# Performance work log

Hardware: AMD Instinct MI355X
Metric: run time of the kernel (lower is better)

## Reference

```python
import jax, jax.numpy as jnp
import numpy as np

N, NEMB, NHID, NCLASS = 8192, 128, 64, 16
NEG_SLOPE = 0.2
NEG_INF = -1e9


def setup_inputs() -> dict:
    key = jax.random.key(0)
    ks = jax.random.split(key, 10)
    x = jax.random.normal(ks[0], (N, NEMB), dtype=jnp.float32)
    adj = (jax.random.uniform(ks[1], (N, N)) < 0.01).astype(jnp.float32)
    adj = jnp.maximum(adj, jnp.eye(N, dtype=jnp.float32))
    s = 1.0 / np.sqrt(NHID)
    W1 = jax.random.uniform(ks[2], (NEMB, NHID), minval=-s, maxval=s, dtype=jnp.float32)
    a1_src = jax.random.uniform(ks[3], (NHID,), minval=-s, maxval=s, dtype=jnp.float32)
    a1_dst = jax.random.uniform(ks[4], (NHID,), minval=-s, maxval=s, dtype=jnp.float32)
    b1 = jnp.zeros((NHID,), dtype=jnp.float32)
    s2 = 1.0 / np.sqrt(NCLASS)
    W2 = jax.random.uniform(ks[5], (NHID, NCLASS), minval=-s2, maxval=s2, dtype=jnp.float32)
    a2_src = jax.random.uniform(ks[6], (NCLASS,), minval=-s2, maxval=s2, dtype=jnp.float32)
    a2_dst = jax.random.uniform(ks[7], (NCLASS,), minval=-s2, maxval=s2, dtype=jnp.float32)
    b2 = jnp.zeros((NCLASS,), dtype=jnp.float32)
    return {"x": x, "adj": adj, "W1": W1, "a1_src": a1_src, "a1_dst": a1_dst,
            "b1": b1, "W2": W2, "a2_src": a2_src, "a2_dst": a2_dst, "b2": b2}


def gat_conv(x, adj_mask, W, a_src, a_dst, b):
    # h: [N, F']
    h = x @ W
    # e_ij = LeakyReLU(a_src . h_i + a_dst . h_j), masked softmax over neighbors j
    alpha_src = h @ a_src  # [N]
    alpha_dst = h @ a_dst  # [N]
    e = jax.nn.leaky_relu(alpha_src[:, None] + alpha_dst[None, :], NEG_SLOPE)
    e = jnp.where(adj_mask, e, NEG_INF)
    attn = jax.nn.softmax(e, axis=-1)  # [N, N]
    out = attn @ h + b
    return jax.nn.elu(out)


def reference(x, adj, W1, a1_src, a1_dst, b1, W2, a2_src, a2_dst, b2):
    mask = adj > 0
    h = gat_conv(x, mask, W1, a1_src, a1_dst, b1)
    out = gat_conv(h, mask, W2, a2_src, a2_dst, b2)
    return out
```

## Files before the change

### kernel.cpp

```cpp
#include <hip/hip_runtime.h>
#include <math.h>

#define NN 8192
#define NEMBD 128
#define NHID 64
#define NCLS 16
#define MAXN 256
#define NEG_SLOPE 0.2f

typedef float f4 __attribute__((ext_vector_type(4)));

__device__ __forceinline__ float wave_max64(float v) {
    v = fmaxf(v, __shfl_xor(v, 1));
    v = fmaxf(v, __shfl_xor(v, 2));
    v = fmaxf(v, __shfl_xor(v, 4));
    v = fmaxf(v, __shfl_xor(v, 8));
    v = fmaxf(v, __shfl_xor(v, 16));
    v = fmaxf(v, __shfl_xor(v, 32));
    return v;
}
__device__ __forceinline__ float wave_sum64(float v) {
    v += __shfl_xor(v, 1);
    v += __shfl_xor(v, 2);
    v += __shfl_xor(v, 4);
    v += __shfl_xor(v, 8);
    v += __shfl_xor(v, 16);
    v += __shfl_xor(v, 32);
    return v;
}

__global__ __launch_bounds__(256) void k1_scan_h1(
    const float* __restrict__ adj, const float* __restrict__ x,
    const float* __restrict__ W1,
    const float* __restrict__ a1s, const float* __restrict__ a1d,
    float* __restrict__ h1, float* __restrict__ als, float* __restrict__ ald,
    int* __restrict__ g_cnt, int* __restrict__ g_nbr) {
    __shared__ int s_idx[4][MAXN];
    int wid = threadIdx.x >> 6, lane = threadIdx.x & 63;
    int row = blockIdx.x * 4 + wid;
    const f4* arow = (const f4*)(adj + (size_t)row * NN);
    const float* xr = x + (size_t)row * NEMBD;
    unsigned long long lt = (1ull << lane) - 1ull;
    int base = 0;
    float hacc = 0.f;
    for (int it = 0; it < NN / 256; ++it) {
        f4 v = __builtin_nontemporal_load(arow + it * 64 + lane);
#pragma unroll
        for (int s = 0; s < 4; ++s) {
            int k = it * 4 + s;
            hacc = fmaf(xr[k], W1[k * NHID + lane], hacc);
        }
#pragma unroll
        for (int s = 0; s < 4; ++s) {
            bool nz = v[s] > 0.f;
            unsigned long long m = __ballot(nz);
            if (nz) {
                int pos = base + __popcll(m & lt);
                if (pos < MAXN) s_idx[wid][pos] = it * 256 + lane * 4 + s;
            }
            base += __popcll(m);
        }
    }
    int cnt = base < MAXN ? base : MAXN;
    if (lane == 0) g_cnt[row] = cnt;
    for (int n = lane; n < cnt; n += 64)
        g_nbr[(size_t)row * MAXN + n] = s_idx[wid][n];
    h1[(size_t)row * NHID + lane] = hacc;
    float ts = wave_sum64(hacc * a1s[lane]);
    float td = wave_sum64(hacc * a1d[lane]);
    if (lane == 0) { als[row] = ts; ald[row] = td; }
}

__global__ __launch_bounds__(256) void k2_attn1_h2(
    const float* __restrict__ h1, const float* __restrict__ als,
    const float* __restrict__ ald, const float* __restrict__ b1,
    const float* __restrict__ W2, const float* __restrict__ a2s,
    const float* __restrict__ a2d,
    const int* __restrict__ g_cnt, const int* __restrict__ g_nbr,
    float* __restrict__ h2, float* __restrict__ als2, float* __restrict__ ald2) {
    __shared__ int   s_idx[4][MAXN];
    __shared__ float s_p[4][MAXN];
    __shared__ float s_h[4][NHID];
    int wid = threadIdx.x >> 6, lane = threadIdx.x & 63;
    int row = blockIdx.x * 4 + wid;
    int cnt = g_cnt[row];
    for (int n = lane; n < cnt; n += 64) s_idx[wid][n] = g_nbr[(size_t)row * MAXN + n];

    float asrow = als[row];
    float mloc = -1e30f;
    for (int n = lane; n < cnt; n += 64) {
        float e = asrow + ald[s_idx[wid][n]];
        e = e > 0.f ? e : NEG_SLOPE * e;
        s_p[wid][n] = e;
        mloc = fmaxf(mloc, e);
    }
    float mrow = wave_max64(mloc);
    float ssum = 0.f;
    for (int n = lane; n < cnt; n += 64) {
        float p = __expf(s_p[wid][n] - mrow);
        s_p[wid][n] = p;
        ssum += p;
    }
    float rinv = 1.f / wave_sum64(ssum);

    int c4 = lane & 15, kk = lane >> 4;
    f4 acc = {0.f, 0.f, 0.f, 0.f};
#pragma unroll 4
    for (int n = kk; n < cnt; n += 4) {
        float p = s_p[wid][n];
        f4 v = ((const f4*)(h1 + (size_t)s_idx[wid][n] * NHID))[c4];
        acc.x = fmaf(p, v.x, acc.x);
        acc.y = fmaf(p, v.y, acc.y);
        acc.z = fmaf(p, v.z, acc.z);
        acc.w = fmaf(p, v.w, acc.w);
    }
    acc.x += __shfl_xor(acc.x, 16); acc.y += __shfl_xor(acc.y, 16);
    acc.z += __shfl_xor(acc.z, 16); acc.w += __shfl_xor(acc.w, 16);
    acc.x += __shfl_xor(acc.x, 32); acc.y += __shfl_xor(acc.y, 32);
    acc.z += __shfl_xor(acc.z, 32); acc.w += __shfl_xor(acc.w, 32);
    if (kk == 0) {
        f4 o;
#pragma unroll
        for (int j = 0; j < 4; ++j) {
            float t = acc[j] * rinv + b1[c4 * 4 + j];
            o[j] = t > 0.f ? t : expm1f(t);
        }
        ((f4*)s_h[wid])[c4] = o;
    }
    __builtin_amdgcn_s_barrier();

    int c = lane & 15, k = lane >> 4;
    float a2 = 0.f;
#pragma unroll
    for (int f = k * 16; f < k * 16 + 16; ++f)
        a2 = fmaf(s_h[wid][f], W2[f * NCLS + c], a2);
    a2 += __shfl_xor(a2, 16);
    a2 += __shfl_xor(a2, 32);
    if (lane < 16) h2[(size_t)row * NCLS + lane] = a2;
    float ts = a2 * a2s[c], td = a2 * a2d[c];
    ts += __shfl_xor(ts, 1); td += __shfl_xor(td, 1);
    ts += __shfl_xor(ts, 2); td += __shfl_xor(td, 2);
    ts += __shfl_xor(ts, 4); td += __shfl_xor(td, 4);
    ts += __shfl_xor(ts, 8); td += __shfl_xor(td, 8);
    if (lane == 0) { als2[row] = ts; ald2[row] = td; }
}

__global__ __launch_bounds__(256) void k3_attn2(
    const float* __restrict__ h2, const float* __restrict__ als2,
    const float* __restrict__ ald2, const float* __restrict__ b2,
    const int* __restrict__ g_cnt, const int* __restrict__ g_nbr,
    float* __restrict__ out) {
    __shared__ int   s_idx[4][MAXN];
    __shared__ float s_p[4][MAXN];
    int wid = threadIdx.x >> 6, lane = threadIdx.x & 63;
    int row = blockIdx.x * 4 + wid;
    int cnt = g_cnt[row];
    for (int n = lane; n < cnt; n += 64) s_idx[wid][n] = g_nbr[(size_t)row * MAXN + n];

    float asrow = als2[row];
    float mloc = -1e30f;
    for (int n = lane; n < cnt; n += 64) {
        float e = asrow + ald2[s_idx[wid][n]];
        e = e > 0.f ? e : NEG_SLOPE * e;
        s_p[wid][n] = e;
        mloc = fmaxf(mloc, e);
    }
    float mrow = wave_max64(mloc);
    float ssum = 0.f;
    for (int n = lane; n < cnt; n += 64) {
        float p = __expf(s_p[wid][n] - mrow);
        s_p[wid][n] = p;
        ssum += p;
    }
    float rinv = 1.f / wave_sum64(ssum);

    int c4 = lane & 3, kk = lane >> 2;
    f4 acc = {0.f, 0.f, 0.f, 0.f};
#pragma unroll 2
    for (int n = kk; n < cnt; n += 16) {
        float p = s_p[wid][n];
        f4 v = ((const f4*)(h2 + (size_t)s_idx[wid][n] * NCLS))[c4];
        acc.x = fmaf(p, v.x, acc.x);
        acc.y = fmaf(p, v.y, acc.y);
        acc.z = fmaf(p, v.z, acc.z);
        acc.w = fmaf(p, v.w, acc.w);
    }
#pragma unroll
    for (int d = 4; d <= 32; d <<= 1) {
        acc.x += __shfl_xor(acc.x, d); acc.y += __shfl_xor(acc.y, d);
        acc.z += __shfl_xor(acc.z, d); acc.w += __shfl_xor(acc.w, d);
    }
    if (kk == 0) {
        f4 o;
#pragma unroll
        for (int j = 0; j < 4; ++j) {
            float t = acc[j] * rinv + b2[c4 * 4 + j];
            o[j] = t > 0.f ? t : expm1f(t);
        }
        ((f4*)(out + (size_t)row * NCLS))[c4] = o;
    }
}

extern "C" void kernel_launch(void* const* d_in, const int* in_sizes, int n_in,
                              void* d_out, int out_size, void* d_ws, size_t ws_size,
                              hipStream_t stream) {
    const float* x   = (const float*)d_in[0];
    const float* adj = (const float*)d_in[1];
    const float* W1  = (const float*)d_in[2];
    const float* a1s = (const float*)d_in[3];
    const float* a1d = (const float*)d_in[4];
    const float* b1  = (const float*)d_in[5];
    const float* W2  = (const float*)d_in[6];
    const float* a2s = (const float*)d_in[7];
    const float* a2d = (const float*)d_in[8];
    const float* b2  = (const float*)d_in[9];
    float* out = (float*)d_out;

    char* ws = (char*)d_ws;
    float* h1   = (float*)(ws + 0);
    float* h2v  = (float*)(ws + 2097152);
    float* als1 = (float*)(ws + 2621440);
    float* ald1 = (float*)(ws + 2654208);
    float* als2 = (float*)(ws + 2686976);
    float* ald2 = (float*)(ws + 2719744);
    int*   gcnt = (int*)  (ws + 2752512);
    int*   gnbr = (int*)  (ws + 2785280);

    dim3 blk(256);
    dim3 grid(NN / 4);
    k1_scan_h1 <<<grid, blk, 0, stream>>>(adj, x, W1, a1s, a1d, h1, als1, ald1, gcnt, gnbr);
    k2_attn1_h2<<<grid, blk, 0, stream>>>(h1, als1, ald1, b1, W2, a2s, a2d, gcnt, gnbr,
                                          h2v, als2, ald2);
    k3_attn2   <<<grid, blk, 0, stream>>>(h2v, als2, ald2, b2, gcnt, gnbr, out);
}
```

Before: 81.06 us.

## Fuse adjacency scan with layer-1 attention and software-pipeline rows per wave

The h1 projection moves into its own small kernel. The adjacency scan is fused with the layer-1 attention and the h2 projection, and each wave now handles 4 rows. While the wave scans one row's adjacency with prefetched chunks, it interleaves the gather-accumulate for the previous row, using double-buffered shared neighbor and probability lists. The aim is to hide the latency of gathering h1 rows behind the 256 MB adjacency stream and to drop one kernel's worth of index reloads. The cost is fewer blocks (512), which may lower the memory parallelism available for streaming the adjacency.

```diff
diff --git a/kernel.cpp b/kernel.cpp
--- a/kernel.cpp
+++ b/kernel.cpp
@@ -7,6 +7,8 @@
 #define NCLS 16
 #define MAXN 256
 #define NEG_SLOPE 0.2f
+#define WPB 4
+#define RPW 4
 
 typedef float f4 __attribute__((ext_vector_type(4)));
 
@@ -29,120 +31,187 @@
     return v;
 }
 
-__global__ __launch_bounds__(256) void k1_scan_h1(
-    const float* __restrict__ adj, const float* __restrict__ x,
-    const float* __restrict__ W1,
+__global__ __launch_bounds__(256) void kA_h1(
+    const float* __restrict__ x, const float* __restrict__ W1,
     const float* __restrict__ a1s, const float* __restrict__ a1d,
-    float* __restrict__ h1, float* __restrict__ als, float* __restrict__ ald,
-    int* __restrict__ g_cnt, int* __restrict__ g_nbr) {
-    __shared__ int s_idx[4][MAXN];
+    float* __restrict__ h1, float* __restrict__ als, float* __restrict__ ald) {
     int wid = threadIdx.x >> 6, lane = threadIdx.x & 63;
     int row = blockIdx.x * 4 + wid;
-    const f4* arow = (const f4*)(adj + (size_t)row * NN);
     const float* xr = x + (size_t)row * NEMBD;
+    float acc = 0.f;
+#pragma unroll 8
+    for (int k = 0; k < NEMBD; ++k)
+        acc = fmaf(xr[k], W1[k * NHID + lane], acc);
+    h1[(size_t)row * NHID + lane] = acc;
+    float ts = wave_sum64(acc * a1s[lane]);
+    float td = wave_sum64(acc * a1d[lane]);
+    if (lane == 0) { als[row] = ts; ald[row] = td; }
+}
+
+__global__ __launch_bounds__(256) void kB_fused(
+    const float* __restrict__ adj, const float* __restrict__ h1,
+    const float* __restrict__ als, const float* __restrict__ ald,
+    const float* __restrict__ b1, const float* __restrict__ W2,
+    const float* __restrict__ a2s, const float* __restrict__ a2d,
+    int* __restrict__ g_cnt, int* __restrict__ g_nbr,
+    float* __restrict__ h2, float* __restrict__ als2, float* __restrict__ ald2) {
+    __shared__ int   S_idx[WPB][2][MAXN];
+    __shared__ float S_p[WPB][2][MAXN];
+    __shared__ float S_h[WPB][NHID];
+    int wid = threadIdx.x >> 6, lane = threadIdx.x & 63;
+    int row0 = (blockIdx.x * WPB + wid) * RPW;
     unsigned long long lt = (1ull << lane) - 1ull;
-    int base = 0;
-    float hacc = 0.f;
-    for (int it = 0; it < NN / 256; ++it) {
-        f4 v = __builtin_nontemporal_load(arow + it * 64 + lane);
-#pragma unroll
-        for (int s = 0; s < 4; ++s) {
-            int k = it * 4 + s;
-            hacc = fmaf(xr[k], W1[k * NHID + lane], hacc);
-        }
-#pragma unroll
-        for (int s = 0; s < 4; ++s) {
-            bool nz = v[s] > 0.f;
-            unsigned long long m = __ballot(nz);
-            if (nz) {
-                int pos = base + __popcll(m & lt);
-                if (pos < MAXN) s_idx[wid][pos] = it * 256 + lane * 4 + s;
-            }
-            base += __popcll(m);
-        }
-    }
-    int cnt = base < MAXN ? base : MAXN;
-    if (lane == 0) g_cnt[row] = cnt;
-    for (int n = lane; n < cnt; n += 64)
-        g_nbr[(size_t)row * MAXN + n] = s_idx[wid][n];
-    h1[(size_t)row * NHID + lane] = hacc;
-    float ts = wave_sum64(hacc * a1s[lane]);
-    float td = wave_sum64(hacc * a1d[lane]);
-    if (lane == 0) { als[row] = ts; ald[row] = td; }
-}
-
-__global__ __launch_bounds__(256) void k2_attn1_h2(
-    const float* __restrict__ h1, const float* __restrict__ als,
-    const float* __restrict__ ald, const float* __restrict__ b1,
-    const float* __restrict__ W2, const float* __restrict__ a2s,
-    const float* __restrict__ a2d,
-    const int* __restrict__ g_cnt, const int* __restrict__ g_nbr,
-    float* __restrict__ h2, float* __restrict__ als2, float* __restrict__ ald2) {
-    __shared__ int   s_idx[4][MAXN];
-    __shared__ float s_p[4][MAXN];
-    __shared__ float s_h[4][NHID];
-    int wid = threadIdx.x >> 6, lane = threadIdx.x & 63;
-    int row = blockIdx.x * 4 + wid;
-    int cnt = g_cnt[row];
-    for (int n = lane; n < cnt; n += 64) s_idx[wid][n] = g_nbr[(size_t)row * MAXN + n];
-
-    float asrow = als[row];
-    float mloc = -1e30f;
-    for (int n = lane; n < cnt; n += 64) {
-        float e = asrow + ald[s_idx[wid][n]];
-        e = e > 0.f ? e : NEG_SLOPE * e;
-        s_p[wid][n] = e;
-        mloc = fmaxf(mloc, e);
-    }
-    float mrow = wave_max64(mloc);
-    float ssum = 0.f;
-    for (int n = lane; n < cnt; n += 64) {
-        float p = __expf(s_p[wid][n] - mrow);
-        s_p[wid][n] = p;
-        ssum += p;
-    }
-    float rinv = 1.f / wave_sum64(ssum);
-
     int c4 = lane & 15, kk = lane >> 4;
+
+    int pcnt = 0, prow = -1;
+    float prinv = 0.f;
     f4 acc = {0.f, 0.f, 0.f, 0.f};
-#pragma unroll 4
-    for (int n = kk; n < cnt; n += 4) {
-        float p = s_p[wid][n];
-        f4 v = ((const f4*)(h1 + (size_t)s_idx[wid][n] * NHID))[c4];
-        acc.x = fmaf(p, v.x, acc.x);
-        acc.y = fmaf(p, v.y, acc.y);
-        acc.z = fmaf(p, v.z, acc.z);
-        acc.w = fmaf(p, v.w, acc.w);
-    }
-    acc.x += __shfl_xor(acc.x, 16); acc.y += __shfl_xor(acc.y, 16);
-    acc.z += __shfl_xor(acc.z, 16); acc.w += __shfl_xor(acc.w, 16);
-    acc.x += __shfl_xor(acc.x, 32); acc.y += __shfl_xor(acc.y, 32);
-    acc.z += __shfl_xor(acc.z, 32); acc.w += __shfl_xor(acc.w, 32);
-    if (kk == 0) {
-        f4 o;
-#pragma unroll
-        for (int j = 0; j < 4; ++j) {
-            float t = acc[j] * rinv + b1[c4 * 4 + j];
-            o[j] = t > 0.f ? t : expm1f(t);
-        }
-        ((f4*)s_h[wid])[c4] = o;
-    }
-    __builtin_amdgcn_s_barrier();
-
-    int c = lane & 15, k = lane >> 4;
-    float a2 = 0.f;
-#pragma unroll
-    for (int f = k * 16; f < k * 16 + 16; ++f)
-        a2 = fmaf(s_h[wid][f], W2[f * NCLS + c], a2);
-    a2 += __shfl_xor(a2, 16);
-    a2 += __shfl_xor(a2, 32);
-    if (lane < 16) h2[(size_t)row * NCLS + lane] = a2;
-    float ts = a2 * a2s[c], td = a2 * a2d[c];
-    ts += __shfl_xor(ts, 1); td += __shfl_xor(td, 1);
-    ts += __shfl_xor(ts, 2); td += __shfl_xor(td, 2);
-    ts += __shfl_xor(ts, 4); td += __shfl_xor(td, 4);
-    ts += __shfl_xor(ts, 8); td += __shfl_xor(td, 8);
-    if (lane == 0) { als2[row] = ts; ald2[row] = td; }
+
+#pragma unroll 1
+    for (int r = 0; r < RPW; ++r) {
+        int row = row0 + r;
+        int buf = r & 1, pb = buf ^ 1;
+        const f4* arow = (const f4*)(adj + (size_t)row * NN);
+        int base = 0;
+        f4 cur0 = __builtin_nontemporal_load(arow + 0 * 64 + lane);
+        f4 cur1 = __builtin_nontemporal_load(arow + 1 * 64 + lane);
+        f4 cur2 = __builtin_nontemporal_load(arow + 2 * 64 + lane);
+        f4 cur3 = __builtin_nontemporal_load(arow + 3 * 64 + lane);
+
+#pragma unroll 1
+        for (int c = 0; c < 8; ++c) {
+            if (r > 0) {
+                int lo = (pcnt * c) >> 3, hi = (pcnt * (c + 1)) >> 3;
+#pragma unroll 2
+                for (int n = lo + kk; n < hi; n += 4) {
+                    float p = S_p[wid][pb][n];
+                    int j = S_idx[wid][pb][n];
+                    f4 v = ((const f4*)(h1 + (size_t)j * NHID))[c4];
+                    acc.x = fmaf(p, v.x, acc.x);
+                    acc.y = fmaf(p, v.y, acc.y);
+                    acc.z = fmaf(p, v.z, acc.z);
+                    acc.w = fmaf(p, v.w, acc.w);
+                }
+            }
+            f4 n0 = {0,0,0,0}, n1 = {0,0,0,0}, n2 = {0,0,0,0}, n3 = {0,0,0,0};
+            if (c < 7) {
+                const f4* p = arow + (c + 1) * 256 + lane;
+                n0 = __builtin_nontemporal_load(p + 0 * 64);
+                n1 = __builtin_nontemporal_load(p + 1 * 64);
+                n2 = __builtin_nontemporal_load(p + 2 * 64);
+                n3 = __builtin_nontemporal_load(p + 3 * 64);
+            }
+#pragma unroll
+            for (int j = 0; j < 4; ++j) {
+                f4 v = (j == 0) ? cur0 : (j == 1) ? cur1 : (j == 2) ? cur2 : cur3;
+                int it = c * 4 + j;
+#pragma unroll
+                for (int s = 0; s < 4; ++s) {
+                    bool nz = v[s] > 0.f;
+                    unsigned long long m = __ballot(nz);
+                    if (nz) {
+                        int pos = base + __popcll(m & lt);
+                        if (pos < MAXN) S_idx[wid][buf][pos] = it * 256 + lane * 4 + s;
+                    }
+                    base += __popcll(m);
+                }
+            }
+            cur0 = n0; cur1 = n1; cur2 = n2; cur3 = n3;
+        }
+
+        int cnt = base < MAXN ? base : MAXN;
+        if (lane == 0) g_cnt[row] = cnt;
+        for (int n = lane; n < cnt; n += 64)
+            g_nbr[(size_t)row * MAXN + n] = S_idx[wid][buf][n];
+
+        if (r > 0) {
+            acc.x += __shfl_xor(acc.x, 16); acc.y += __shfl_xor(acc.y, 16);
+            acc.z += __shfl_xor(acc.z, 16); acc.w += __shfl_xor(acc.w, 16);
+            acc.x += __shfl_xor(acc.x, 32); acc.y += __shfl_xor(acc.y, 32);
+            acc.z += __shfl_xor(acc.z, 32); acc.w += __shfl_xor(acc.w, 32);
+            if (kk == 0) {
+                f4 o;
+#pragma unroll
+                for (int j = 0; j < 4; ++j) {
+                    float t = acc[j] * prinv + b1[c4 * 4 + j];
+                    o[j] = t > 0.f ? t : expm1f(t);
+                }
+                ((f4*)S_h[wid])[c4] = o;
+            }
+            float a2 = 0.f;
+#pragma unroll
+            for (int f = kk * 16; f < kk * 16 + 16; ++f)
+                a2 = fmaf(S_h[wid][f], W2[f * NCLS + c4], a2);
+            a2 += __shfl_xor(a2, 16);
+            a2 += __shfl_xor(a2, 32);
+            if (lane < 16) h2[(size_t)prow * NCLS + lane] = a2;
+            float ts = a2 * a2s[c4], td = a2 * a2d[c4];
+            ts += __shfl_xor(ts, 1); td += __shfl_xor(td, 1);
+            ts += __shfl_xor(ts, 2); td += __shfl_xor(td, 2);
+            ts += __shfl_xor(ts, 4); td += __shfl_xor(td, 4);
+            ts += __shfl_xor(ts, 8); td += __shfl_xor(td, 8);
+            if (lane == 0) { als2[prow] = ts; ald2[prow] = td; }
+            acc = (f4){0.f, 0.f, 0.f, 0.f};
+        }
+
+        float asr = als[row];
+        float mloc = -1e30f;
+        for (int n = lane; n < cnt; n += 64) {
+            float e = asr + ald[S_idx[wid][buf][n]];
+            e = e > 0.f ? e : NEG_SLOPE * e;
+            S_p[wid][buf][n] = e;
+            mloc = fmaxf(mloc, e);
+        }
+        float mrow = wave_max64(mloc);
+        float ssum = 0.f;
+        for (int n = lane; n < cnt; n += 64) {
+            float p = __expf(S_p[wid][buf][n] - mrow);
+            S_p[wid][buf][n] = p;
+            ssum += p;
+        }
+        prinv = 1.f / wave_sum64(ssum);
+        pcnt = cnt; prow = row;
+    }
+
+    {
+        int pb = (RPW - 1) & 1;
+#pragma unroll 2
+        for (int n = kk; n < pcnt; n += 4) {
+            float p = S_p[wid][pb][n];
+            int j = S_idx[wid][pb][n];
+            f4 v = ((const f4*)(h1 + (size_t)j * NHID))[c4];
+            acc.x = fmaf(p, v.x, acc.x);
+            acc.y = fmaf(p, v.y, acc.y);
+            acc.z = fmaf(p, v.z, acc.z);
+            acc.w = fmaf(p, v.w, acc.w);
+        }
+        acc.x += __shfl_xor(acc.x, 16); acc.y += __shfl_xor(acc.y, 16);
+        acc.z += __shfl_xor(acc.z, 16); acc.w += __shfl_xor(acc.w, 16);
+        acc.x += __shfl_xor(acc.x, 32); acc.y += __shfl_xor(acc.y, 32);
+        acc.z += __shfl_xor(acc.z, 32); acc.w += __shfl_xor(acc.w, 32);
+        if (kk == 0) {
+            f4 o;
+#pragma unroll
+            for (int j = 0; j < 4; ++j) {
+                float t = acc[j] * prinv + b1[c4 * 4 + j];
+                o[j] = t > 0.f ? t : expm1f(t);
+            }
+            ((f4*)S_h[wid])[c4] = o;
+        }
+        float a2 = 0.f;
+#pragma unroll
+        for (int f = kk * 16; f < kk * 16 + 16; ++f)
+            a2 = fmaf(S_h[wid][f], W2[f * NCLS + c4], a2);
+        a2 += __shfl_xor(a2, 16);
+        a2 += __shfl_xor(a2, 32);
+        if (lane < 16) h2[(size_t)prow * NCLS + lane] = a2;
+        float ts = a2 * a2s[c4], td = a2 * a2d[c4];
+        ts += __shfl_xor(ts, 1); td += __shfl_xor(td, 1);
+        ts += __shfl_xor(ts, 2); td += __shfl_xor(td, 2);
+        ts += __shfl_xor(ts, 4); td += __shfl_xor(td, 4);
+        ts += __shfl_xor(ts, 8); td += __shfl_xor(td, 8);
+        if (lane == 0) { als2[prow] = ts; ald2[prow] = td; }
+    }
 }
 
 __global__ __launch_bounds__(256) void k3_attn2(
@@ -227,9 +296,8 @@
     int*   gnbr = (int*)  (ws + 2785280);
 
     dim3 blk(256);
-    dim3 grid(NN / 4);
-    k1_scan_h1 <<<grid, blk, 0, stream>>>(adj, x, W1, a1s, a1d, h1, als1, ald1, gcnt, gnbr);
-    k2_attn1_h2<<<grid, blk, 0, stream>>>(h1, als1, ald1, b1, W2, a2s, a2d, gcnt, gnbr,
-                                          h2v, als2, ald2);
-    k3_attn2   <<<grid, blk, 0, stream>>>(h2v, als2, ald2, b2, gcnt, gnbr, out);
-}
+    kA_h1   <<<dim3(NN / 4), blk, 0, stream>>>(x, W1, a1s, a1d, h1, als1, ald1);
+    kB_fused<<<dim3(NN / (WPB * RPW)), blk, 0, stream>>>(
+        adj, h1, als1, ald1, b1, W2, a2s, a2d, gcnt, gnbr, h2v, als2, ald2);
+    k3_attn2<<<dim3(NN / 4), blk, 0, stream>>>(h2v, als2, ald2, b2, gcnt, gnbr, out);
+}
```

Result: slower. 118.0 us (+45.6%).
